# Optimization experiments

Measured on AMD Instinct MI355X. Metric: run time of the kernel, lower is better.

The kernel has to match this reference:

```python
import jax, jax.numpy as jnp
import numpy as np

HIDDEN = 1024
BATCH = 8192
N_STEPS = 50


def setup_inputs() -> dict:
    key = jax.random.key(0)
    k1, k2, k3 = jax.random.split(key, 3)
    x0 = jax.random.normal(k1, (HIDDEN, BATCH), dtype=jnp.float32)
    W = jax.random.normal(k2, (HIDDEN, HIDDEN), dtype=jnp.float32) * (1.0 / np.sqrt(HIDDEN))
    b = jax.random.normal(k3, (HIDDEN, 1), dtype=jnp.float32)
    t0 = jnp.zeros((), dtype=jnp.float32)
    t1 = jnp.ones((), dtype=jnp.float32)
    return {"x0": x0, "t0": t0, "t1": t1, "W": W, "b": b}


def reference(x0, t0, t1, W, b):
    # Euler integration: x_{i+1} = x_i + h * (W @ x_i + b), h = (t1 - t0) / N
    h = (t1 - t0) / N_STEPS

    def step(x, _):
        x = x + h * (W @ x + b)  # b [H,1] broadcasts over batch
        return x, None

    x_final, _ = jax.lax.scan(step, x0, None, length=N_STEPS)
    return x_final
```

## Files before the change

### kernel.cpp

```cpp
#include <hip/hip_runtime.h>

#define H 1024
#define HH (H * H)
#define BATCH 8192
#define NSTEPS 50

typedef __attribute__((ext_vector_type(8))) short bf16x8;
typedef __attribute__((ext_vector_type(4))) float f32x4;

__device__ __forceinline__ void split2(float a, unsigned short& h, unsigned short& l)
{
    unsigned u = __float_as_uint(a);
    float r = a - __uint_as_float(u & 0xFFFF0000u);
    h = (unsigned short)(u >> 16);
    l = (unsigned short)((__float_as_uint(r) + 0x8000u) >> 16);
}
__device__ __forceinline__ unsigned short rnd_bf16(float a)
{
    return (unsigned short)((__float_as_uint(a) + 0x8000u) >> 16);
}
__device__ __forceinline__ float bf2f(unsigned short s)
{
    return __uint_as_float(((unsigned)s) << 16);
}
__device__ __forceinline__ void gload16(const void* g, void* l)
{
    __builtin_amdgcn_global_load_lds(
        (const __attribute__((address_space(1))) void*)g,
        (__attribute__((address_space(3))) void*)l, 16, 0, 0);
}

__global__ void setup_k(const float* __restrict__ W, const float* __restrict__ bvec,
                        const float* __restrict__ t0, const float* __restrict__ t1,
                        unsigned short* __restrict__ Aplanes,
                        float* __restrict__ cv, float* __restrict__ v0)
{
    __shared__ unsigned short th[64][68], tl[64][68];
    const float h = (t1[0] - t0[0]) / (float)NSTEPS;
    const int bid = blockIdx.x, tid = threadIdx.x;
    const int rb = (bid >> 4) * 64, cb = (bid & 15) * 64;
    const int row = tid >> 2, c16 = (tid & 3) * 16;

    unsigned short* Ahi  = Aplanes;
    unsigned short* Alo  = Aplanes + HH;
    unsigned short* AhiT = Aplanes + 2 * HH;
    unsigned short* AloT = Aplanes + 3 * HH;

    {
        const float* wsrc = &W[(size_t)(rb + row) * H + cb + c16];
        bf16x8 hv[2], lv[2];
        #pragma unroll
        for (int q = 0; q < 16; ++q) {
            const float a = h * wsrc[q] + ((rb + row) == (cb + c16 + q) ? 1.0f : 0.0f);
            unsigned short hh, ll;
            split2(a, hh, ll);
            hv[q >> 3][q & 7] = (short)hh;
            lv[q >> 3][q & 7] = (short)ll;
            th[row][c16 + q] = hh;
            tl[row][c16 + q] = ll;
        }
        *(bf16x8*)&Ahi[(size_t)(rb + row) * H + cb + c16] = hv[0];
        *(bf16x8*)&Ahi[(size_t)(rb + row) * H + cb + c16 + 8] = hv[1];
        *(bf16x8*)&Alo[(size_t)(rb + row) * H + cb + c16] = lv[0];
        *(bf16x8*)&Alo[(size_t)(rb + row) * H + cb + c16 + 8] = lv[1];
    }
    __syncthreads();
    {
        bf16x8 hv[2], lv[2];
        #pragma unroll
        for (int q = 0; q < 16; ++q) {
            hv[q >> 3][q & 7] = (short)th[c16 + q][row];
            lv[q >> 3][q & 7] = (short)tl[c16 + q][row];
        }
        *(bf16x8*)&AhiT[(size_t)(cb + row) * H + rb + c16] = hv[0];
        *(bf16x8*)&AhiT[(size_t)(cb + row) * H + rb + c16 + 8] = hv[1];
        *(bf16x8*)&AloT[(size_t)(cb + row) * H + rb + c16] = lv[0];
        *(bf16x8*)&AloT[(size_t)(cb + row) * H + rb + c16 + 8] = lv[1];
    }
    if (bid == 0) {
        #pragma unroll
        for (int rep = 0; rep < 4; ++rep) {
            const int i = tid + rep * 256;
            const float v = h * bvec[i];
            cv[i] = v; v0[i] = v;
        }
    }
}

template<bool WRITE_T, bool DO_X, bool PR>
__launch_bounds__(512)
__global__ void chain_fused_k(const unsigned short* __restrict__ Lhi,
                              const unsigned short* __restrict__ Llo,
                              const unsigned short* __restrict__ RThi,
                              const unsigned short* __restrict__ RTlo,
                              unsigned short* __restrict__ Qhi,
                              unsigned short* __restrict__ Qlo,
                              unsigned short* __restrict__ QhiT,
                              unsigned short* __restrict__ QloT,
                              const float* __restrict__ vin,
                              const float* __restrict__ addv,
                              float* __restrict__ vout,
                              const float* __restrict__ X,
                              unsigned short* __restrict__ XhiT)
{
    __shared__ unsigned short sA[2][2][2][64][32];
    __shared__ unsigned short sB[2][2][2][64][32];

    const int tid = threadIdx.x;
    const int bid = blockIdx.x;
    const int wave = tid >> 6, lane = tid & 63;

    if (DO_X && bid >= 272) {
        float (*ts)[65] = (float(*)[65])&sA[0][0][0][0][0];
        const int tile = bid - 272;
        const int n0x = (tile >> 4) * 64, k0x = (tile & 15) * 64;
        #pragma unroll
        for (int p = 0; p < 2; ++p) {
            const int kr = p * 32 + (tid >> 4);
            const int c4 = (tid & 15) * 4;
            const float4 v = *(const float4*)&X[(size_t)(k0x + kr) * BATCH + n0x + c4];
            ts[kr][c4 + 0] = v.x; ts[kr][c4 + 1] = v.y;
            ts[kr][c4 + 2] = v.z; ts[kr][c4 + 3] = v.w;
        }
        __syncthreads();
        {
            const int n = tid >> 3;
            const int kc = (tid & 7) * 8;
            bf16x8 hv;
            #pragma unroll
            for (int q = 0; q < 8; ++q)
                hv[q] = (short)rnd_bf16(ts[kc + q][n]);
            *(bf16x8*)&XhiT[(size_t)(n0x + n) * H + k0x + kc] = hv;
        }
        return;
    }

    if (bid >= 256) {
        const int rowbase = (bid - 256) * 64 + wave * 8;
        const float4* xq = (const float4*)vin + lane * 4;
        float4 xv[4];
        #pragma unroll
        for (int q = 0; q < 4; ++q) xv[q] = xq[q];
        #pragma unroll
        for (int rr = 0; rr < 8; ++rr) {
            const int row = rowbase + rr;
            const unsigned short* mh = Lhi + (size_t)row * H + lane * 16;
            const unsigned short* ml = Llo + (size_t)row * H + lane * 16;
            bf16x8 h0 = *(const bf16x8*)&mh[0];
            bf16x8 h1 = *(const bf16x8*)&mh[8];
            bf16x8 l0 = *(const bf16x8*)&ml[0];
            bf16x8 l1 = *(const bf16x8*)&ml[8];
            float s = 0.0f;
            #pragma unroll
            for (int q = 0; q < 8; ++q) {
                const float m0v = bf2f((unsigned short)h0[q]) + bf2f((unsigned short)l0[q]);
                const float m1v = bf2f((unsigned short)h1[q]) + bf2f((unsigned short)l1[q]);
                const float* xf = (const float*)xv;
                s = fmaf(m0v, xf[q], s);
                s = fmaf(m1v, xf[8 + q], s);
            }
            #pragma unroll
            for (int off = 32; off; off >>= 1)
                s += __shfl_down(s, off, 64);
            if (lane == 0) vout[row] = addv[row] + s;
        }
        return;
    }

    const int lg = lane >> 4, lm = lane & 15;
    const int half = wave >> 2;
    const int wq = wave & 3;
    const int wr2 = (wq >> 1) * 32, wc2 = (wq & 1) * 32;
    const int xcd = bid & 7;
    const int idx0 = bid >> 3;
    const int mt = (xcd >> 1) * 4 + (idx0 & 3);
    const int nt = (xcd & 1) * 8 + (idx0 >> 2);
    const int m0 = mt * 64, n0 = nt * 64;

    f32x4 acc[2][2] = {};

    #define CSTAGE(tt, b) do {                                                   \
        _Pragma("unroll")                                                        \
        for (int it = 0; it < 4; ++it) {                                         \
            const int idx = tid + it * 512;                                      \
            const int mat = idx >> 10, kh = (idx >> 9) & 1;                      \
            const int plane = (idx >> 8) & 1;                                    \
            const int row = (idx >> 2) & 63, kc = idx & 3;                       \
            const int ks = kc ^ ((row >> 1) & 3);                                \
            const unsigned short* g = mat ? (plane ? RTlo : RThi)                \
                                          : (plane ? Llo : Lhi);                 \
            const int rb = mat ? n0 : m0;                                        \
            unsigned short* d = mat ? &sB[b][kh][plane][row][kc * 8]             \
                                    : &sA[b][kh][plane][row][kc * 8];            \
            gload16(g + (size_t)(rb + row) * H + kh * 512 + (tt) * 32 + ks * 8, d); \
        }                                                                        \
    } while (0)

    CSTAGE(0, 0);
    __syncthreads();
    int buf = 0;
    for (int t = 0; t < 16; ++t) {
        if (t + 1 < 16) CSTAGE(t + 1, buf ^ 1);
        bf16x8 ah[2], al[2], bh[2], bl[2];
        #pragma unroll
        for (int i = 0; i < 2; ++i) {
            const int row = wr2 + i * 16 + lm;
            const int sl = lg ^ ((row >> 1) & 3);
            ah[i] = *(const bf16x8*)&sA[buf][half][0][row][sl * 8];
            al[i] = *(const bf16x8*)&sA[buf][half][1][row][sl * 8];
            const int rn = wc2 + i * 16 + lm;
            const int sn = lg ^ ((rn >> 1) & 3);
            bh[i] = *(const bf16x8*)&sB[buf][half][0][rn][sn * 8];
            bl[i] = *(const bf16x8*)&sB[buf][half][1][rn][sn * 8];
        }
        #pragma unroll
        for (int i = 0; i < 2; ++i)
            #pragma unroll
            for (int j = 0; j < 2; ++j) {
                acc[i][j] = __builtin_amdgcn_mfma_f32_16x16x32_bf16(ah[i], bh[j], acc[i][j], 0, 0, 0);
                acc[i][j] = __builtin_amdgcn_mfma_f32_16x16x32_bf16(ah[i], bl[j], acc[i][j], 0, 0, 0);
                acc[i][j] = __builtin_amdgcn_mfma_f32_16x16x32_bf16(al[i], bh[j], acc[i][j], 0, 0, 0);
            }
        __syncthreads();
        buf ^= 1;
    }
    #undef CSTAGE

    float* red = (float*)&sA[0][0][0][0][0];
    const int ridx = wq * 64 + lane;
    if (half == 1) {
        float* dst = red + (size_t)ridx * 17;
        #pragma unroll
        for (int i = 0; i < 2; ++i)
            #pragma unroll
            for (int j = 0; j < 2; ++j)
                *(f32x4*)&dst[(i * 2 + j) * 4] = acc[i][j];
    }
    __syncthreads();
    if (half == 0) {
        const float* src = red + (size_t)ridx * 17;
        #pragma unroll
        for (int i = 0; i < 2; ++i)
            #pragma unroll
            for (int j = 0; j < 2; ++j) {
                const f32x4 p = *(const f32x4*)&src[(i * 2 + j) * 4];
                acc[i][j] += p;
            }
        #pragma unroll
        for (int i = 0; i < 2; ++i) {
            const int row0 = m0 + wr2 + i * 16 + lg * 4;
            #pragma unroll
            for (int j = 0; j < 2; ++j) {
                const int col = n0 + wc2 + j * 16 + lm;
                if (PR) {
                    #pragma unroll
                    for (int r = 0; r < 4; ++r)
                        Qhi[(size_t)(row0 + r) * H + col] = rnd_bf16(acc[i][j][r]);
                } else {
                    unsigned short hs[4], ls[4];
                    #pragma unroll
                    for (int r = 0; r < 4; ++r) {
                        split2(acc[i][j][r], hs[r], ls[r]);
                        Qhi[(size_t)(row0 + r) * H + col] = hs[r];
                        Qlo[(size_t)(row0 + r) * H + col] = ls[r];
                    }
                    if (WRITE_T) {
                        ushort4 th, tl;
                        th.x = hs[0]; th.y = hs[1]; th.z = hs[2]; th.w = hs[3];
                        tl.x = ls[0]; tl.y = ls[1]; tl.z = ls[2]; tl.w = ls[3];
                        *(ushort4*)&QhiT[(size_t)col * H + row0] = th;
                        *(ushort4*)&QloT[(size_t)col * H + row0] = tl;
                    }
                }
            }
        }
    }
}

__launch_bounds__(256)
__global__ void big_gemm1_k(const unsigned short* __restrict__ Pr,
                            const unsigned short* __restrict__ XhiT,
                            float* __restrict__ C, const float* __restrict__ bias)
{
    __shared__ unsigned short sA[2][128][32];
    __shared__ unsigned short sB[2][128][32];

    const int tid = threadIdx.x;
    const int wave = tid >> 6, lane = tid & 63;
    const int lg = lane >> 4, lm = lane & 15;
    const int wr2 = (wave >> 1) * 64;
    const int wc2 = (wave & 1) * 64;
    const int bid = blockIdx.x;
    const int l = bid >> 3;
    const int m0 = (l & 7) * 128;
    const int n0 = ((bid & 7) * 8 + (l >> 3)) * 128;

    f32x4 acc[4][4] = {};

    #define BSTAGE(tt, b) do {                                                   \
        _Pragma("unroll")                                                        \
        for (int it = 0; it < 2; ++it) {                                         \
            const int idx = tid + it * 256;                                      \
            const int row = idx >> 2, kc = idx & 3;                              \
            const int ks = kc ^ ((row >> 1) & 3);                                \
            const size_t go = (size_t)(tt) * 32 + ks * 8;                        \
            gload16(Pr   + (size_t)(m0 + row) * H + go, &sA[b][row][kc * 8]);    \
            gload16(XhiT + (size_t)(n0 + row) * H + go, &sB[b][row][kc * 8]);    \
        }                                                                        \
    } while (0)

    BSTAGE(0, 0);
    __syncthreads();
    int buf = 0;
    for (int t = 0; t < 32; ++t) {
        if (t + 1 < 32) BSTAGE(t + 1, buf ^ 1);
        bf16x8 ah[4], bh[4];
        #pragma unroll
        for (int i = 0; i < 4; ++i) {
            const int row = wr2 + i * 16 + lm;
            const int sl = lg ^ ((row >> 1) & 3);
            ah[i] = *(const bf16x8*)&sA[buf][row][sl * 8];
            const int rn = wc2 + i * 16 + lm;
            const int sn = lg ^ ((rn >> 1) & 3);
            bh[i] = *(const bf16x8*)&sB[buf][rn][sn * 8];
        }
        __builtin_amdgcn_s_setprio(1);
        #pragma unroll
        for (int i = 0; i < 4; ++i)
            #pragma unroll
            for (int j = 0; j < 4; ++j)
                acc[i][j] = __builtin_amdgcn_mfma_f32_16x16x32_bf16(ah[i], bh[j], acc[i][j], 0, 0, 0);
        __builtin_amdgcn_s_setprio(0);
        __syncthreads();
        buf ^= 1;
    }
    #undef BSTAGE

    #pragma unroll
    for (int i = 0; i < 4; ++i) {
        const int row0 = m0 + wr2 + i * 16 + lg * 4;
        #pragma unroll
        for (int r = 0; r < 4; ++r) {
            const float bv = bias[row0 + r];
            float* dst = &C[(size_t)(row0 + r) * BATCH + n0 + wc2 + lm];
            #pragma unroll
            for (int j = 0; j < 4; ++j)
                dst[j * 16] = acc[i][j][r] + bv;
        }
    }
}

#define PADK 40

__launch_bounds__(256)
__global__ void big_gemm_k(const unsigned short* __restrict__ Ahi_g,
                           const unsigned short* __restrict__ Alo_g,
                           const float* __restrict__ X, float* __restrict__ C,
                           const float* __restrict__ bias)
{
    __shared__ unsigned short Ahi[128][PADK], Alo[128][PADK];
    __shared__ unsigned short Bhi[128][PADK], Blo[128][PADK];

    const int tid = threadIdx.x;
    const int wave = tid >> 6;
    const int lane = tid & 63;
    const int wr = (wave >> 1) * 64;
    const int wc = (wave & 1) * 64;
    const int m0 = blockIdx.y * 128;
    const int n0 = blockIdx.x * 128;
    const int lg = lane >> 4;
    const int lm = lane & 15;

    f32x4 acc[4][4] = {};

    for (int k0 = 0; k0 < H; k0 += 32) {
        #pragma unroll
        for (int a2 = 0; a2 < 2; ++a2) {
            const int id = tid + a2 * 256;
            const int row = id >> 2;
            const int ko = id & 3;
            const size_t g = (size_t)(m0 + row) * H + k0 + ko * 8;
            *(bf16x8*)&Ahi[row][ko * 8] = *(const bf16x8*)&Ahi_g[g];
            *(bf16x8*)&Alo[row][ko * 8] = *(const bf16x8*)&Alo_g[g];
        }
        #pragma unroll
        for (int a2 = 0; a2 < 2; ++a2) {
            const int id = tid + a2 * 256;
            const int n = id & 127;
            const int ko = id >> 7;
            const float* src = &X[(size_t)(k0 + ko * 8) * BATCH + n0 + n];
            bf16x8 bh, bl;
            #pragma unroll
            for (int i = 0; i < 8; ++i) {
                unsigned short hh, ll;
                split2(src[(size_t)i * BATCH], hh, ll);
                bh[i] = (short)hh;
                bl[i] = (short)ll;
            }
            *(bf16x8*)&Bhi[n][ko * 8] = bh;
            *(bf16x8*)&Blo[n][ko * 8] = bl;
        }
        __syncthreads();

        bf16x8 ah[4], al[4], bh[4], bl[4];
        #pragma unroll
        for (int i = 0; i < 4; ++i) {
            const int m = wr + i * 16 + lm;
            ah[i] = *(const bf16x8*)&Ahi[m][lg * 8];
            al[i] = *(const bf16x8*)&Alo[m][lg * 8];
            const int n = wc + i * 16 + lm;
            bh[i] = *(const bf16x8*)&Bhi[n][lg * 8];
            bl[i] = *(const bf16x8*)&Blo[n][lg * 8];
        }
        #pragma unroll
        for (int i = 0; i < 4; ++i)
            #pragma unroll
            for (int j = 0; j < 4; ++j) {
                acc[i][j] = __builtin_amdgcn_mfma_f32_16x16x32_bf16(ah[i], bh[j], acc[i][j], 0, 0, 0);
                acc[i][j] = __builtin_amdgcn_mfma_f32_16x16x32_bf16(ah[i], bl[j], acc[i][j], 0, 0, 0);
                acc[i][j] = __builtin_amdgcn_mfma_f32_16x16x32_bf16(al[i], bh[j], acc[i][j], 0, 0, 0);
            }
        __syncthreads();
    }

    #pragma unroll
    for (int i = 0; i < 4; ++i) {
        const int rowb = m0 + wr + i * 16 + lg * 4;
        #pragma unroll
        for (int r = 0; r < 4; ++r) {
            const float bv = bias[rowb + r];
            float* dst = &C[(size_t)(rowb + r) * BATCH + n0 + wc + lm];
            #pragma unroll
            for (int j = 0; j < 4; ++j)
                dst[j * 16] = acc[i][j][r] + bv;
        }
    }
}

extern "C" void kernel_launch(void* const* d_in, const int* in_sizes, int n_in,
                              void* d_out, int out_size, void* d_ws, size_t ws_size,
                              hipStream_t stream)
{
    const float* x0 = (const float*)d_in[0];
    const float* t0 = (const float*)d_in[1];
    const float* t1 = (const float*)d_in[2];
    const float* W  = (const float*)d_in[3];
    const float* bb = (const float*)d_in[4];
    float* out = (float*)d_out;

    unsigned short* Aplanes = (unsigned short*)d_ws;
    unsigned short* Ahi  = Aplanes;
    unsigned short* Alo  = Aplanes + HH;
    float* cv = (float*)(Aplanes + 4 * HH);
    float* v0 = cv + H;
    float* v1 = v0 + H;

    const size_t xtoff = (size_t)16 * 1024 * 1024;
    const bool useXT = ws_size >= xtoff + (size_t)BATCH * H * sizeof(unsigned short);
    unsigned short* XhiT = (unsigned short*)((char*)d_ws + xtoff);

    unsigned short* PA = (unsigned short*)d_out;
    unsigned short* PB = PA + (size_t)4 * HH;

    setup_k<<<256, 256, 0, stream>>>(W, bb, t0, t1, Aplanes, cv, v0);

    const int seq[7] = {0, 1, 0, 0, 0, 1, 0};
    unsigned short* cur = Ahi;
    float* vin = v0;
    float* vout = v1;
    for (int s = 0; s < 7; ++s) {
        const unsigned short* L  = seq[s] ? Ahi : cur;
        const unsigned short* Ll = seq[s] ? Alo : cur + HH;
        const float* addv = seq[s] ? cv : vin;
        if (s == 0) {
            unsigned short* nxt = PA;
            if (useXT) {
                chain_fused_k<true, true, false><<<2320, 512, 0, stream>>>(
                    L, Ll, cur + 2 * HH, cur + 3 * HH,
                    nxt, nxt + HH, nxt + 2 * HH, nxt + 3 * HH,
                    vin, addv, vout, x0, XhiT);
            } else {
                chain_fused_k<true, false, false><<<272, 512, 0, stream>>>(
                    L, Ll, cur + 2 * HH, cur + 3 * HH,
                    nxt, nxt + HH, nxt + 2 * HH, nxt + 3 * HH,
                    vin, addv, vout, nullptr, nullptr);
            }
            cur = nxt;
        } else if (s < 6) {
            unsigned short* nxt = (s & 1) ? PB : PA;
            chain_fused_k<true, false, false><<<272, 512, 0, stream>>>(
                L, Ll, cur + 2 * HH, cur + 3 * HH,
                nxt, nxt + HH, nxt + 2 * HH, nxt + 3 * HH,
                vin, addv, vout, nullptr, nullptr);
            cur = nxt;
        } else if (useXT) {
            chain_fused_k<false, false, true><<<272, 512, 0, stream>>>(
                L, Ll, cur + 2 * HH, cur + 3 * HH,
                Ahi, nullptr, nullptr, nullptr,
                vin, addv, vout, nullptr, nullptr);
            cur = Ahi;
        } else {
            chain_fused_k<false, false, false><<<272, 512, 0, stream>>>(
                L, Ll, cur + 2 * HH, cur + 3 * HH,
                Ahi, Alo, nullptr, nullptr,
                vin, addv, vout, nullptr, nullptr);
            cur = Ahi;
        }
        float* tv = vin; vin = vout; vout = tv;
    }

    if (useXT) {
        big_gemm1_k<<<512, 256, 0, stream>>>(Ahi, XhiT, out, vin);
    } else {
        big_gemm_k<<<dim3(BATCH / 128, H / 128), 256, 0, stream>>>(
            Ahi, Alo, x0, out, vin);
    }
}
```

Before: 157.2 us.

## Triple-buffer final GEMM loads and skip unused normal-layout chain writes

The final big GEMM moves from a double-buffered LDS pipeline to a three-stage one. It prefetches two tiles ahead and uses explicit vmcnt waits plus raw barriers instead of __syncthreads, so loads overlap the MFMA work better. Separately, a new WRITE_N template flag lets chain steps whose output is only consumed as the left operand in transposed form skip writing the normal-layout hi/lo planes, which cuts global store traffic. The risks are correctness if a skipped plane is later read, and higher LDS use per block.

```diff
diff --git a/kernel.cpp b/kernel.cpp
--- a/kernel.cpp
+++ b/kernel.cpp
@@ -29,6 +29,8 @@
         (const __attribute__((address_space(1))) void*)g,
         (__attribute__((address_space(3))) void*)l, 16, 0, 0);
 }
+#define VMCNT(n) asm volatile("s_waitcnt vmcnt(" #n ")" ::: "memory")
+#define RBAR() do { __builtin_amdgcn_s_barrier(); __builtin_amdgcn_sched_barrier(0); } while (0)
 
 __global__ void setup_k(const float* __restrict__ W, const float* __restrict__ bvec,
                         const float* __restrict__ t0, const float* __restrict__ t1,
@@ -87,7 +89,7 @@
     }
 }
 
-template<bool WRITE_T, bool DO_X, bool PR>
+template<bool WRITE_N, bool WRITE_T, bool DO_X, bool PR>
 __launch_bounds__(512)
 __global__ void chain_fused_k(const unsigned short* __restrict__ Lhi,
                               const unsigned short* __restrict__ Llo,
@@ -261,8 +263,10 @@
                     #pragma unroll
                     for (int r = 0; r < 4; ++r) {
                         split2(acc[i][j][r], hs[r], ls[r]);
-                        Qhi[(size_t)(row0 + r) * H + col] = hs[r];
-                        Qlo[(size_t)(row0 + r) * H + col] = ls[r];
+                        if (WRITE_N) {
+                            Qhi[(size_t)(row0 + r) * H + col] = hs[r];
+                            Qlo[(size_t)(row0 + r) * H + col] = ls[r];
+                        }
                     }
                     if (WRITE_T) {
                         ushort4 th, tl;
@@ -282,8 +286,8 @@
                             const unsigned short* __restrict__ XhiT,
                             float* __restrict__ C, const float* __restrict__ bias)
 {
-    __shared__ unsigned short sA[2][128][32];
-    __shared__ unsigned short sB[2][128][32];
+    __shared__ unsigned short sA[3][128][32];
+    __shared__ unsigned short sB[3][128][32];
 
     const int tid = threadIdx.x;
     const int wave = tid >> 6, lane = tid & 63;
@@ -310,20 +314,24 @@
     } while (0)
 
     BSTAGE(0, 0);
-    __syncthreads();
-    int buf = 0;
+    BSTAGE(1, 1);
+    VMCNT(2);
+    RBAR();
+
+    #pragma unroll
     for (int t = 0; t < 32; ++t) {
-        if (t + 1 < 32) BSTAGE(t + 1, buf ^ 1);
+        const int b = t % 3;
         bf16x8 ah[4], bh[4];
         #pragma unroll
         for (int i = 0; i < 4; ++i) {
             const int row = wr2 + i * 16 + lm;
             const int sl = lg ^ ((row >> 1) & 3);
-            ah[i] = *(const bf16x8*)&sA[buf][row][sl * 8];
+            ah[i] = *(const bf16x8*)&sA[b][row][sl * 8];
             const int rn = wc2 + i * 16 + lm;
             const int sn = lg ^ ((rn >> 1) & 3);
-            bh[i] = *(const bf16x8*)&sB[buf][rn][sn * 8];
-        }
+            bh[i] = *(const bf16x8*)&sB[b][rn][sn * 8];
+        }
+        if (t + 2 < 32) BSTAGE(t + 2, (t + 2) % 3);
         __builtin_amdgcn_s_setprio(1);
         #pragma unroll
         for (int i = 0; i < 4; ++i)
@@ -331,8 +339,9 @@
             for (int j = 0; j < 4; ++j)
                 acc[i][j] = __builtin_amdgcn_mfma_f32_16x16x32_bf16(ah[i], bh[j], acc[i][j], 0, 0, 0);
         __builtin_amdgcn_s_setprio(0);
-        __syncthreads();
-        buf ^= 1;
+        if (t < 30) VMCNT(2);
+        else if (t == 30) VMCNT(0);
+        if (t < 31) RBAR();
     }
     #undef BSTAGE
 
@@ -475,32 +484,39 @@
         if (s == 0) {
             unsigned short* nxt = PA;
             if (useXT) {
-                chain_fused_k<true, true, false><<<2320, 512, 0, stream>>>(
+                chain_fused_k<false, true, true, false><<<2320, 512, 0, stream>>>(
                     L, Ll, cur + 2 * HH, cur + 3 * HH,
                     nxt, nxt + HH, nxt + 2 * HH, nxt + 3 * HH,
                     vin, addv, vout, x0, XhiT);
             } else {
-                chain_fused_k<true, false, false><<<272, 512, 0, stream>>>(
+                chain_fused_k<false, true, false, false><<<272, 512, 0, stream>>>(
                     L, Ll, cur + 2 * HH, cur + 3 * HH,
                     nxt, nxt + HH, nxt + 2 * HH, nxt + 3 * HH,
                     vin, addv, vout, nullptr, nullptr);
             }
             cur = nxt;
+        } else if (s == 4) {
+            unsigned short* nxt = PA;
+            chain_fused_k<false, true, false, false><<<272, 512, 0, stream>>>(
+                L, Ll, cur + 2 * HH, cur + 3 * HH,
+                nxt, nxt + HH, nxt + 2 * HH, nxt + 3 * HH,
+                vin, addv, vout, nullptr, nullptr);
+            cur = nxt;
         } else if (s < 6) {
             unsigned short* nxt = (s & 1) ? PB : PA;
-            chain_fused_k<true, false, false><<<272, 512, 0, stream>>>(
+            chain_fused_k<true, true, false, false><<<272, 512, 0, stream>>>(
                 L, Ll, cur + 2 * HH, cur + 3 * HH,
                 nxt, nxt + HH, nxt + 2 * HH, nxt + 3 * HH,
                 vin, addv, vout, nullptr, nullptr);
             cur = nxt;
         } else if (useXT) {
-            chain_fused_k<false, false, true><<<272, 512, 0, stream>>>(
+            chain_fused_k<false, false, false, true><<<272, 512, 0, stream>>>(
                 L, Ll, cur + 2 * HH, cur + 3 * HH,
                 Ahi, nullptr, nullptr, nullptr,
                 vin, addv, vout, nullptr, nullptr);
             cur = Ahi;
         } else {
-            chain_fused_k<false, false, false><<<272, 512, 0, stream>>>(
+            chain_fused_k<true, false, false, false><<<272, 512, 0, stream>>>(
                 L, Ll, cur + 2 * HH, cur + 3 * HH,
                 Ahi, Alo, nullptr, nullptr,
                 vin, addv, vout, nullptr, nullptr);
```

Measured after the change: 150.8 us. 1.04x faster.
